# Kernel tuning notes

Measured on AMD Instinct MI355X. Metric: run time of the kernel, lower is better.

Reference implementation:

```python
import jax, jax.numpy as jnp
import numpy as np

NUM_EMBEDDINGS = 8192
EMBEDDING_DIM = 256


def setup_inputs() -> dict:
    key = jax.random.key(0)
    kx, kw = jax.random.split(key)
    x = jax.random.normal(kx, (16384, EMBEDDING_DIM), dtype=jnp.float32)
    # nn.Embedding weight initialized uniform(-1/K, 1/K)
    bound = 1.0 / NUM_EMBEDDINGS
    weight = jax.random.uniform(kw, (NUM_EMBEDDINGS, EMBEDDING_DIM),
                                dtype=jnp.float32, minval=-bound, maxval=bound)
    return {"x": x, "weight": weight}


def reference(x, weight):
    # flatten to (N, D)
    flat_x = x.reshape(-1, EMBEDDING_DIM)
    distances = (jnp.sum(flat_x * flat_x, axis=1, keepdims=True)
                 + jnp.sum(weight * weight, axis=1)
                 - 2.0 * jnp.matmul(flat_x, weight.T))
    encoding_indices = jnp.argmin(distances, axis=1)  # (N,)
    quantized = weight[encoding_indices].reshape(x.shape)
    return quantized, encoding_indices
```

## Files before the change

kernel.cpp:

```cpp
#include <hip/hip_runtime.h>
#include <hip/hip_bf16.h>

#define NROWS 16384
#define NCODES 8192
#define DIM 256
#define BM 128
#define SPLITS 2
#define CPB (NCODES / SPLITS)
#define CAP 32
#define MARGIND 1.7e-4f

#define WFRAG_BLOCKS 1024
#define SQ_BLOCKS 1536

typedef __attribute__((ext_vector_type(8))) short bf16x8;
typedef __attribute__((ext_vector_type(4))) float f32x4;

__device__ inline unsigned short f2bf(float f) {
    union { __hip_bfloat16 h; unsigned short u; } cv;
    cv.h = __float2bfloat16(f);
    return cv.u;
}
__device__ inline unsigned f2ord(float f) {
    unsigned u = __float_as_uint(f);
    return u ^ ((u >> 31) ? 0xFFFFFFFFu : 0x80000000u);
}
__device__ inline float ord2f(unsigned u) {
    unsigned v = (u & 0x80000000u) ? (u ^ 0x80000000u) : ~u;
    return __uint_as_float(v);
}

__device__ inline void gload16(const unsigned short* g, unsigned short* l) {
    __builtin_amdgcn_global_load_lds(
        (__attribute__((address_space(1))) void*)g,
        (__attribute__((address_space(3))) void*)l, 16, 0, 0);
}

__global__ __launch_bounds__(256)
void prep_kernel(const float* __restrict__ x, const float* __restrict__ w,
                 unsigned short* __restrict__ whf,
                 float* __restrict__ xsq, float* __restrict__ wsq,
                 unsigned long long* __restrict__ best64g) {
    if (blockIdx.x < WFRAG_BLOCKS) {
        int tid = blockIdx.x * 256 + threadIdx.x;
        int L = tid & 63;
        int rest = tid >> 6;
        int k32 = rest & 7;
        int c16 = rest >> 3;
        int code = c16 * 16 + (L & 15);
        int k = k32 * 32 + (L >> 4) * 8;
        const float4* p = reinterpret_cast<const float4*>(w + (size_t)code * DIM + k);
        float4 u0 = p[0], u1 = p[1];
        unsigned short tmp[8];
        tmp[0] = f2bf(u0.x); tmp[1] = f2bf(u0.y); tmp[2] = f2bf(u0.z); tmp[3] = f2bf(u0.w);
        tmp[4] = f2bf(u1.x); tmp[5] = f2bf(u1.y); tmp[6] = f2bf(u1.z); tmp[7] = f2bf(u1.w);
        *reinterpret_cast<uint4*>(whf + (size_t)tid * 8) = *reinterpret_cast<uint4*>(tmp);
    } else {
        int blk = blockIdx.x - WFRAG_BLOCKS;
        int row = blk * 16 + (threadIdx.x >> 4);
        int c = threadIdx.x & 15;
        int j = c & 7, h = c >> 3;
        const float* src = (row < NROWS) ? (x + (size_t)row * DIM)
                                         : (w + (size_t)(row - NROWS) * DIM);
        const float* base = src + h * 128 + j;
        float r = 0.0f;
        #pragma unroll
        for (int g = 0; g < 16; ++g) {
            float v = base[g * 8];
            r = __fadd_rn(r, __fmul_rn(v, v));
        }
        float t;
        t = __shfl_xor(r, 1, 64); r = __fadd_rn(r, t);
        t = __shfl_xor(r, 2, 64); r = __fadd_rn(r, t);
        t = __shfl_xor(r, 4, 64); r = __fadd_rn(r, t);
        t = __shfl_xor(r, 8, 64); r = __fadd_rn(r, t);
        if (c == 0) {
            if (row < NROWS) xsq[row] = r;
            else wsq[row - NROWS] = r;
        }
        if (c == 1 && row < NROWS) best64g[row] = 0xFFFFFFFFFFFFFFFFULL;
    }
}

__global__ __launch_bounds__(512, 2)
void vq_main(const float* __restrict__ x, const float* __restrict__ w,
             const unsigned short* __restrict__ whf,
             const float* __restrict__ wsq, const float* __restrict__ xsq,
             unsigned long long* __restrict__ best64g) {
    __shared__ unsigned short afrag[8 * 8 * 64 * 8];
    __shared__ unsigned short bstage[2 * 8 * 4 * 64 * 8];
    __shared__ unsigned rowmax[BM];
    __shared__ int cnt[BM];
    __shared__ int cand[BM][CAP];
    __shared__ int ovf_list[BM];
    __shared__ int ovf_n;

    const int tid = threadIdx.x;
    const int lane = tid & 63;
    const int wv = tid >> 6;
    const int lm = lane & 15;
    const int lq = lane >> 4;

    const int blk = blockIdx.x;
    const int xcd = blk & 7;
    const int split = xcd & 1;
    const int rowGroup = (xcd >> 1) * 32 + (blk >> 3);
    const int rowBase = rowGroup * BM;
    const int codeBase = split * CPB;
    const int codeBase16 = codeBase >> 4;
    const int waveCode16 = codeBase16 + wv * 32;

    if (tid < BM) { rowmax[tid] = 0u; cnt[tid] = 0; }
    if (tid == 0) ovf_n = 0;

    unsigned short* bpriv = bstage + wv * 2048;

    {
        const unsigned short* src =
            whf + (size_t)waveCode16 * 4096 + lane * 8;
        #pragma unroll
        for (int cf = 0; cf < 4; ++cf)
            gload16(src + cf * 4096, bpriv + cf * 512);
    }

    {
        const int rg = wv;
        const float* xr = x + (size_t)(rowBase + rg * 16 + lm) * DIM + lq * 8;
        #pragma unroll
        for (int k32 = 0; k32 < 8; ++k32) {
            float4 u0 = *reinterpret_cast<const float4*>(xr + k32 * 32);
            float4 u1 = *reinterpret_cast<const float4*>(xr + k32 * 32 + 4);
            unsigned short t8[8];
            t8[0] = f2bf(u0.x); t8[1] = f2bf(u0.y); t8[2] = f2bf(u0.z); t8[3] = f2bf(u0.w);
            t8[4] = f2bf(u1.x); t8[5] = f2bf(u1.y); t8[6] = f2bf(u1.z); t8[7] = f2bf(u1.w);
            *reinterpret_cast<uint4*>(afrag + ((rg * 8 + k32) * 64 + lane) * 8) =
                *reinterpret_cast<uint4*>(t8);
        }
    }
    __syncthreads();

    const unsigned short* afb = afrag + (size_t)lane * 8;

    #pragma unroll 1
    for (int p = 0; p < 8; ++p) {
        const int pbase16 = waveCode16 + p * 4;

        f32x4 acc[8][4];
        #pragma unroll
        for (int rg = 0; rg < 8; ++rg)
            #pragma unroll
            for (int cf = 0; cf < 4; ++cf)
                acc[rg][cf] = (f32x4){0.f, 0.f, 0.f, 0.f};

        #pragma unroll 1
        for (int s = 0; s < 8; ++s) {
            const int g = p * 8 + s;
            if (g < 63) {
                const int gn = g + 1;
                const int pn = gn >> 3, sn = gn & 7;
                const unsigned short* src =
                    whf + (size_t)(waveCode16 + pn * 4) * 4096 + sn * 512 + lane * 8;
                unsigned short* dst = bpriv + ((s & 1) ^ 1) * 16384;
                #pragma unroll
                for (int cf = 0; cf < 4; ++cf)
                    gload16(src + cf * 4096, dst + cf * 512);
                asm volatile("s_waitcnt vmcnt(4)" ::: "memory");
            } else {
                asm volatile("s_waitcnt vmcnt(0)" ::: "memory");
            }
            __builtin_amdgcn_sched_barrier(0);

            const unsigned short* bbase = bpriv + (s & 1) * 16384 + lane * 8;
            bf16x8 bb[4];
            #pragma unroll
            for (int cf = 0; cf < 4; ++cf)
                bb[cf] = *reinterpret_cast<const bf16x8*>(bbase + cf * 512);
            bf16x8 a[8];
            #pragma unroll
            for (int rg = 0; rg < 8; ++rg)
                a[rg] = *reinterpret_cast<const bf16x8*>(afb + (rg * 8 + s) * 512);
            #pragma unroll
            for (int cf = 0; cf < 4; ++cf)
                #pragma unroll
                for (int rg = 0; rg < 8; ++rg)
                    acc[rg][cf] = __builtin_amdgcn_mfma_f32_16x16x32_bf16(
                        bb[cf], a[rg], acc[rg][cf], 0, 0, 0);
        }

        #pragma unroll
        for (int rg = 0; rg < 8; ++rg) {
            float m = -__builtin_huge_valf();
            #pragma unroll
            for (int cf = 0; cf < 4; ++cf)
                #pragma unroll
                for (int r = 0; r < 4; ++r)
                    m = fmaxf(m, acc[rg][cf][r]);
            float rm = fmaxf(m, __shfl_xor(m, 16, 64));
            rm = fmaxf(rm, __shfl_xor(rm, 32, 64));
            const int row = rg * 16 + lm;
            if (lq == 0) atomicMax(&rowmax[row], f2ord(rm));
            float limit = ord2f(rowmax[row]) - MARGIND;
            if (m >= limit) {
                #pragma unroll
                for (int cf = 0; cf < 4; ++cf)
                    #pragma unroll
                    for (int r = 0; r < 4; ++r) {
                        if (acc[rg][cf][r] >= limit) {
                            int pos = atomicAdd(&cnt[row], 1);
                            if (pos < CAP)
                                cand[row][pos] = (pbase16 + cf) * 16 + lq * 4 + r;
                        }
                    }
            }
        }
    }
    __syncthreads();

    if (tid < BM && cnt[tid] > CAP) {
        int i = atomicAdd(&ovf_n, 1);
        ovf_list[i] = tid;
    }
    __syncthreads();

    for (int slot = tid; slot < BM * CAP; slot += 512) {
        int row = slot / CAP, pos = slot - (slot / CAP) * CAP;
        int n = cnt[row] < CAP ? cnt[row] : CAP;
        if (pos < n) {
            int c = cand[row][pos];
            const float* xr = x + (size_t)(rowBase + row) * DIM;
            const float* wr = w + (size_t)c * DIM;
            float d = 0.f;
            for (int k = 0; k < DIM; k += 4) {
                float4 a = *reinterpret_cast<const float4*>(xr + k);
                float4 b = *reinterpret_cast<const float4*>(wr + k);
                d = fmaf(a.x, b.x, d);
                d = fmaf(a.y, b.y, d);
                d = fmaf(a.z, b.z, d);
                d = fmaf(a.w, b.w, d);
            }
            float t1 = __fadd_rn(xsq[rowBase + row], wsq[c]);
            float s = __fsub_rn(t1, __fadd_rn(d, d));
            unsigned long long key =
                ((unsigned long long)__float_as_uint(s) << 32) | (unsigned)c;
            atomicMin(best64g + rowBase + row, key);
        }
    }

    #pragma unroll 1
    for (int i = 0; i < ovf_n; ++i) {
        const int row = ovf_list[i];
        const float* xr = x + (size_t)(rowBase + row) * DIM;
        const float xq = xsq[rowBase + row];
        unsigned long long best = 0xFFFFFFFFFFFFFFFFULL;
        #pragma unroll 1
        for (int t0 = tid; t0 < CPB; t0 += 1024) {
            int ca = codeBase + t0;
            int cb = codeBase + t0 + 512;
            const float* wa = w + (size_t)ca * DIM;
            const float* wb = w + (size_t)cb * DIM;
            float da = 0.f, db = 0.f;
            #pragma unroll
            for (int k = 0; k < DIM; k += 4) {
                float4 av  = *reinterpret_cast<const float4*>(xr + k);
                float4 b4a = *reinterpret_cast<const float4*>(wa + k);
                float4 b4b = *reinterpret_cast<const float4*>(wb + k);
                da = fmaf(av.x, b4a.x, da); da = fmaf(av.y, b4a.y, da);
                da = fmaf(av.z, b4a.z, da); da = fmaf(av.w, b4a.w, da);
                db = fmaf(av.x, b4b.x, db); db = fmaf(av.y, b4b.y, db);
                db = fmaf(av.z, b4b.z, db); db = fmaf(av.w, b4b.w, db);
            }
            float sa = __fsub_rn(__fadd_rn(xq, wsq[ca]), __fadd_rn(da, da));
            float sb = __fsub_rn(__fadd_rn(xq, wsq[cb]), __fadd_rn(db, db));
            unsigned long long ka =
                ((unsigned long long)__float_as_uint(sa) << 32) | (unsigned)ca;
            unsigned long long kb =
                ((unsigned long long)__float_as_uint(sb) << 32) | (unsigned)cb;
            best = best < ka ? best : ka;
            best = best < kb ? best : kb;
        }
        #pragma unroll
        for (int msk = 32; msk >= 1; msk >>= 1) {
            unsigned long long o = __shfl_xor(best, msk, 64);
            best = best < o ? best : o;
        }
        if (lane == 0) atomicMin(best64g + rowBase + row, best);
    }
}

__global__ __launch_bounds__(256)
void out_kernel(const float* __restrict__ w,
                const unsigned long long* __restrict__ best64g,
                float* __restrict__ out_q, float* __restrict__ out_idx) {
    int r = blockIdx.x * 4 + (threadIdx.x >> 6);
    int lane = threadIdx.x & 63;
    unsigned long long key = best64g[r];
    int idx = (int)(key & 0xFFFFFFFFu);
    float4 v = reinterpret_cast<const float4*>(w + (size_t)idx * DIM)[lane];
    reinterpret_cast<float4*>(out_q + (size_t)r * DIM)[lane] = v;
    if (lane == 0) out_idx[r] = (float)idx;
}

extern "C" void kernel_launch(void* const* d_in, const int* in_sizes, int n_in,
                              void* d_out, int out_size, void* d_ws, size_t ws_size,
                              hipStream_t stream) {
    const float* x = (const float*)d_in[0];
    const float* w = (const float*)d_in[1];
    float* out_q = (float*)d_out;
    float* out_idx = (float*)d_out + (size_t)NROWS * DIM;

    unsigned short* whf = (unsigned short*)d_ws;
    float* wsq = (float*)((char*)d_ws + (size_t)NCODES * DIM * 2);
    float* xsq = wsq + NCODES;
    unsigned long long* best64g = (unsigned long long*)(xsq + NROWS);

    prep_kernel<<<WFRAG_BLOCKS + SQ_BLOCKS, 256, 0, stream>>>(x, w, whf, xsq, wsq, best64g);
    vq_main<<<(NROWS / BM) * SPLITS, 512, 0, stream>>>(x, w, whf, wsq, xsq, best64g);
    out_kernel<<<NROWS / 4, 256, 0, stream>>>(w, best64g, out_q, out_idx);
}
```

Baseline: 253.8 us.

## Load codebook fragments directly into registers instead of LDS staging

The main kernel no longer stages codebook bf16 fragments through per-wave LDS double buffers via global_load_lds. Each wave now loads B fragments straight into a two-deep register double buffer with the k-loop fully unrolled, which frees the bstage LDS allocation. Candidate capacity CAP drops from 32 to 24, further cutting shared memory. The norm prep path now reads rows into shared memory with coalesced float4 loads before reducing. The trade-off is more register pressure and reliance on the compiler to schedule global-load latency around the MFMAs, plus a higher risk of candidate overflow.

Measured after the change: 342.7 us. +35.0%, slower.

```diff
diff --git a/kernel.cpp b/kernel.cpp
--- a/kernel.cpp
+++ b/kernel.cpp
@@ -7,7 +7,7 @@
 #define BM 128
 #define SPLITS 2
 #define CPB (NCODES / SPLITS)
-#define CAP 32
+#define CAP 24
 #define MARGIND 1.7e-4f
 
 #define WFRAG_BLOCKS 1024
@@ -28,12 +28,6 @@
 __device__ inline float ord2f(unsigned u) {
     unsigned v = (u & 0x80000000u) ? (u ^ 0x80000000u) : ~u;
     return __uint_as_float(v);
-}
-
-__device__ inline void gload16(const unsigned short* g, unsigned short* l) {
-    __builtin_amdgcn_global_load_lds(
-        (__attribute__((address_space(1))) void*)g,
-        (__attribute__((address_space(3))) void*)l, 16, 0, 0);
 }
 
 __global__ __launch_bounds__(256)
@@ -56,13 +50,25 @@
         tmp[4] = f2bf(u1.x); tmp[5] = f2bf(u1.y); tmp[6] = f2bf(u1.z); tmp[7] = f2bf(u1.w);
         *reinterpret_cast<uint4*>(whf + (size_t)tid * 8) = *reinterpret_cast<uint4*>(tmp);
     } else {
+        __shared__ float xs[16][260];
         int blk = blockIdx.x - WFRAG_BLOCKS;
-        int row = blk * 16 + (threadIdx.x >> 4);
+        int rowBase = blk * 16;
+        #pragma unroll
+        for (int it = 0; it < 4; ++it) {
+            int idx = threadIdx.x + it * 256;
+            int r = idx >> 6;
+            int c4 = idx & 63;
+            int grow = rowBase + r;
+            const float* src = (grow < NROWS) ? (x + (size_t)grow * DIM)
+                                              : (w + (size_t)(grow - NROWS) * DIM);
+            float4 v = *reinterpret_cast<const float4*>(src + c4 * 4);
+            *reinterpret_cast<float4*>(&xs[r][c4 * 4]) = v;
+        }
+        __syncthreads();
+        int row = rowBase + (threadIdx.x >> 4);
         int c = threadIdx.x & 15;
         int j = c & 7, h = c >> 3;
-        const float* src = (row < NROWS) ? (x + (size_t)row * DIM)
-                                         : (w + (size_t)(row - NROWS) * DIM);
-        const float* base = src + h * 128 + j;
+        const float* base = &xs[threadIdx.x >> 4][h * 128 + j];
         float r = 0.0f;
         #pragma unroll
         for (int g = 0; g < 16; ++g) {
@@ -88,7 +94,6 @@
              const float* __restrict__ wsq, const float* __restrict__ xsq,
              unsigned long long* __restrict__ best64g) {
     __shared__ unsigned short afrag[8 * 8 * 64 * 8];
-    __shared__ unsigned short bstage[2 * 8 * 4 * 64 * 8];
     __shared__ unsigned rowmax[BM];
     __shared__ int cnt[BM];
     __shared__ int cand[BM][CAP];
@@ -108,20 +113,9 @@
     const int rowBase = rowGroup * BM;
     const int codeBase = split * CPB;
     const int codeBase16 = codeBase >> 4;
-    const int waveCode16 = codeBase16 + wv * 32;
 
     if (tid < BM) { rowmax[tid] = 0u; cnt[tid] = 0; }
     if (tid == 0) ovf_n = 0;
-
-    unsigned short* bpriv = bstage + wv * 2048;
-
-    {
-        const unsigned short* src =
-            whf + (size_t)waveCode16 * 4096 + lane * 8;
-        #pragma unroll
-        for (int cf = 0; cf < 4; ++cf)
-            gload16(src + cf * 4096, bpriv + cf * 512);
-    }
 
     {
         const int rg = wv;
@@ -140,10 +134,12 @@
     __syncthreads();
 
     const unsigned short* afb = afrag + (size_t)lane * 8;
+    const int waveCode16 = codeBase16 + wv * 32;
 
     #pragma unroll 1
     for (int p = 0; p < 8; ++p) {
         const int pbase16 = waveCode16 + p * 4;
+        const unsigned short* wpass = whf + (size_t)pbase16 * 4096 + lane * 8;
 
         f32x4 acc[8][4];
         #pragma unroll
@@ -152,39 +148,30 @@
             for (int cf = 0; cf < 4; ++cf)
                 acc[rg][cf] = (f32x4){0.f, 0.f, 0.f, 0.f};
 
-        #pragma unroll 1
-        for (int s = 0; s < 8; ++s) {
-            const int g = p * 8 + s;
-            if (g < 63) {
-                const int gn = g + 1;
-                const int pn = gn >> 3, sn = gn & 7;
-                const unsigned short* src =
-                    whf + (size_t)(waveCode16 + pn * 4) * 4096 + sn * 512 + lane * 8;
-                unsigned short* dst = bpriv + ((s & 1) ^ 1) * 16384;
+        bf16x8 bb[2][4];
+        #pragma unroll
+        for (int cf = 0; cf < 4; ++cf)
+            bb[0][cf] = *reinterpret_cast<const bf16x8*>(wpass + cf * 4096);
+
+        #pragma unroll
+        for (int k32 = 0; k32 < 8; ++k32) {
+            const int cur = k32 & 1;
+            if (k32 < 7) {
                 #pragma unroll
                 for (int cf = 0; cf < 4; ++cf)
-                    gload16(src + cf * 4096, dst + cf * 512);
-                asm volatile("s_waitcnt vmcnt(4)" ::: "memory");
-            } else {
-                asm volatile("s_waitcnt vmcnt(0)" ::: "memory");
+                    bb[cur ^ 1][cf] = *reinterpret_cast<const bf16x8*>(
+                        wpass + cf * 4096 + (k32 + 1) * 512);
             }
-            __builtin_amdgcn_sched_barrier(0);
-
-            const unsigned short* bbase = bpriv + (s & 1) * 16384 + lane * 8;
-            bf16x8 bb[4];
-            #pragma unroll
-            for (int cf = 0; cf < 4; ++cf)
-                bb[cf] = *reinterpret_cast<const bf16x8*>(bbase + cf * 512);
             bf16x8 a[8];
             #pragma unroll
             for (int rg = 0; rg < 8; ++rg)
-                a[rg] = *reinterpret_cast<const bf16x8*>(afb + (rg * 8 + s) * 512);
+                a[rg] = *reinterpret_cast<const bf16x8*>(afb + (rg * 8 + k32) * 512);
             #pragma unroll
             for (int cf = 0; cf < 4; ++cf)
                 #pragma unroll
                 for (int rg = 0; rg < 8; ++rg)
                     acc[rg][cf] = __builtin_amdgcn_mfma_f32_16x16x32_bf16(
-                        bb[cf], a[rg], acc[rg][cf], 0, 0, 0);
+                        bb[cur][cf], a[rg], acc[rg][cf], 0, 0, 0);
         }
 
         #pragma unroll
```
